# Optimization experiments

Hardware: AMD Instinct MI355X
Metric: run time of the kernel (lower is better)

## Reference

```python
import jax, jax.numpy as jnp
import numpy as np
from jax import lax

V_VOX, T_PTS, D, H, W = 12000, 35, 10, 200, 176
EPS = 1e-5


def _bn(x, g, b, axes, shape):
    m = x.mean(axes, keepdims=True)
    v = x.var(axes, keepdims=True)  # biased var, matches torch BN training stats
    return g.reshape(shape) * (x - m) * lax.rsqrt(v + EPS) + b.reshape(shape)


def _conv3d(x, w, b):
    y = lax.conv_general_dilated(x, w, (1, 1, 1), 'SAME',
                                 dimension_numbers=('NCDHW', 'OIDHW', 'NCDHW'))
    return y + b[None, :, None, None, None]


def _conv2d(x, w, b):
    y = lax.conv_general_dilated(x, w, (1, 1), 'SAME',
                                 dimension_numbers=('NCHW', 'OIHW', 'NCHW'))
    return y + b[None, :, None, None]


def setup_inputs() -> dict:
    key = jax.random.key(0)
    ks = jax.random.split(key, 12)
    voxels = jax.random.normal(ks[0], (1, V_VOX, T_PTS, 4), jnp.float32)
    # unique voxel coordinates (the torch loop overwrites on duplicates; unique avoids ambiguity)
    rng = np.random.default_rng(0)
    flat = rng.choice(D * H * W, size=V_VOX, replace=False)
    z = flat // (H * W); rem = flat % (H * W)
    coords = jnp.asarray(np.stack([z, rem // W, rem % W], axis=1), dtype=jnp.int32)
    s = 0.05
    p = dict(
        w_lin=jax.random.normal(ks[1], (32, 4), jnp.float32) * s,
        b_lin=jnp.zeros((32,), jnp.float32),
        g_bn0=jnp.ones((32,), jnp.float32), be_bn0=jnp.zeros((32,), jnp.float32),
        w_c3a=jax.random.normal(ks[2], (64, 32, 3, 3, 3), jnp.float32) * s,
        b_c3a=jnp.zeros((64,), jnp.float32),
        g_bn1=jnp.ones((64,), jnp.float32), be_bn1=jnp.zeros((64,), jnp.float32),
        w_c3b=jax.random.normal(ks[3], (64, 64, 3, 3, 3), jnp.float32) * s,
        b_c3b=jnp.zeros((64,), jnp.float32),
        g_bn2=jnp.ones((64,), jnp.float32), be_bn2=jnp.zeros((64,), jnp.float32),
        w_r1=jax.random.normal(ks[4], (128, 64, 3, 3), jnp.float32) * s,
        b_r1=jnp.zeros((128,), jnp.float32),
        w_r2=jax.random.normal(ks[5], (8, 128, 1, 1), jnp.float32) * s,
        b_r2=jnp.zeros((8,), jnp.float32),
    )
    return dict(voxels=voxels, coords=coords, **p)


def reference(voxels, coords, w_lin, b_lin, g_bn0, be_bn0,
              w_c3a, b_c3a, g_bn1, be_bn1, w_c3b, b_c3b, g_bn2, be_bn2,
              w_r1, b_r1, w_r2, b_r2):
    B, V, T, C = voxels.shape
    # SimpleVFE: linear -> BN1d (batch stats) -> relu -> max over points
    h = voxels.reshape(B * V * T, C) @ w_lin.T + b_lin          # [BVT,32]
    h = jax.nn.relu(_bn(h, g_bn0, be_bn0, 0, (1, 32)))
    feats = h.reshape(B, V, T, 32).max(axis=2)                  # [B,V,32]
    # fused scatter into dense volume (replaces per-voxel python loop)
    volume = jnp.zeros((B, 32, D, H, W), voxels.dtype)
    volume = volume.at[0, :, coords[:, 0], coords[:, 1], coords[:, 2]].set(feats[0])
    # 3D backbone
    x = jax.nn.relu(_bn(_conv3d(volume, w_c3a, b_c3a), g_bn1, be_bn1, (0, 2, 3, 4), (1, 64, 1, 1, 1)))
    x = jax.nn.relu(_bn(_conv3d(x, w_c3b, b_c3b), g_bn2, be_bn2, (0, 2, 3, 4), (1, 64, 1, 1, 1)))
    x = x.mean(axis=2)                                          # collapse depth -> [B,64,H,W]
    # RPN head
    out = _conv2d(jax.nn.relu(_conv2d(x, w_r1, b_r1)), w_r2, b_r2)  # [B,8,H,W]
    box = jnp.concatenate([out[:, 0:3], jnp.exp(out[:, 3:6]),
                           jnp.tanh(out[:, 6:7]), jax.nn.sigmoid(out[:, 7:8])], axis=1)
    return box
```

## Files before the change

kernel.cpp:

```cpp
#include <hip/hip_runtime.h>
#include <math.h>

#define V_VOX 12000
#define T_PTS 35
#define DD 10
#define HH 200
#define WW 176
#define EPSV 1e-5f

#define DP 12
#define HP 202
#define WP 178
#define PPLN (HP * WP)
#define PVOX (DP * PPLN)
#define NPIX (DD * HH * WW)
#define HWPIX (HH * WW)

typedef _Float16 half_t;
typedef _Float16 f16x8 __attribute__((ext_vector_type(8)));
typedef float f32x4 __attribute__((ext_vector_type(4)));

#define WPA_OFF 0
#define WPB_OFF 110592
#define WPR1_OFF 331776
#define STATS_OFF 479232
#define FEATS_OFF 483328
#define VOLP_OFF 2019328
#define X1P_OFF 29633536
#define Y_OFF 84861952
#define PLANE_OFF 129917952
#define R1OUT_OFF 134520320

#define S_BN0S 0
#define S_BN0Q 32
#define S_BN1S 64
#define S_BN1Q 128
#define S_BN2S 192
#define S_BN2Q 256
#define C0A 320
#define C0B 352
#define C1A 384
#define C1B 448
#define C2A 512
#define C2B 576

__device__ __forceinline__ void gload16(const half_t* g, half_t* l) {
    __builtin_amdgcn_global_load_lds(
        (const __attribute__((address_space(1))) void*)g,
        (__attribute__((address_space(3))) void*)l, 16, 0, 0);
}

__global__ void k_pack(const float* __restrict__ w, half_t* __restrict__ wp,
                       int IC, int NT, int OC) {
    int id = blockIdx.x * 256 + threadIdx.x;
    int OCT = OC >> 4, KH = IC >> 5;
    int total = NT * KH * OCT * 512;
    if (id >= total) return;
    int j = id & 7;
    int lane = (id >> 3) & 63;
    int rest = id >> 9;
    int ot = rest % OCT; rest /= OCT;
    int kh = rest % KH;
    int tap = rest / KH;
    int oc = ot * 16 + (lane & 15);
    int ic = kh * 32 + (lane >> 4) * 8 + j;
    wp[id] = (half_t)w[(oc * IC + ic) * NT + tap];
}

__global__ void k_vfe_stats(const float4* __restrict__ vox, const float* __restrict__ w_lin,
                            const float* __restrict__ b_lin, float* __restrict__ S) {
    int tid = blockIdx.x * 256 + threadIdx.x;
    int c = threadIdx.x & 31;
    float4 w = ((const float4*)w_lin)[c];
    float bl = b_lin[c];
    float s = 0.f, q = 0.f;
    const int np = V_VOX * T_PTS;
    int stride = gridDim.x * 8;
    for (int p = tid >> 5; p < np; p += stride) {
        float4 v = vox[p];
        float d = v.x * w.x + v.y * w.y + v.z * w.z + v.w * w.w + bl;
        s += d;
        q += d * d;
    }
    s += __shfl_xor(s, 32);
    q += __shfl_xor(q, 32);
    if ((threadIdx.x & 63) < 32) {
        atomicAdd(&S[S_BN0S + c], s);
        atomicAdd(&S[S_BN0Q + c], q);
    }
}

__global__ void k_bn_final(const float* __restrict__ ss, const float* __restrict__ sq,
                           const float* __restrict__ g, const float* __restrict__ be,
                           float* __restrict__ ca, float* __restrict__ cb, int C, float invN) {
    int c = threadIdx.x;
    if (c >= C) return;
    float m = ss[c] * invN;
    float v = sq[c] * invN - m * m;
    float a = g[c] * rsqrtf(v + EPSV);
    ca[c] = a;
    cb[c] = be[c] - m * a;
}

__global__ void k_vfe_max(const float4* __restrict__ vox, const float* __restrict__ w_lin,
                          const float* __restrict__ b_lin, const float* __restrict__ ca,
                          const float* __restrict__ cb, float* __restrict__ feats) {
    int id = blockIdx.x * 256 + threadIdx.x;
    if (id >= V_VOX * 32) return;
    int c = id & 31;
    int v = id >> 5;
    float4 w = ((const float4*)w_lin)[c];
    float bl = b_lin[c], A = ca[c], B = cb[c];
    float m = 0.f;
    for (int t = 0; t < T_PTS; t++) {
        float4 p = vox[v * T_PTS + t];
        float d = p.x * w.x + p.y * w.y + p.z * w.z + p.w * w.w + bl;
        m = fmaxf(m, A * d + B);
    }
    feats[id] = m;
}

__global__ void k_scatter(const float* __restrict__ feats, const int* __restrict__ coords,
                          half_t* __restrict__ volp) {
    int id = blockIdx.x * 256 + threadIdx.x;
    if (id >= V_VOX * 32) return;
    int c = id & 31;
    int v = id >> 5;
    int z = coords[v * 3 + 0];
    int y = coords[v * 3 + 1];
    int x = coords[v * 3 + 2];
    volp[(((z + 1) * HP + (y + 1)) * WP + (x + 1)) * 32 + c] = (half_t)feats[id];
}

template <int KH, int DZ, int OCTP, bool RELU, bool STATS>
__global__ __launch_bounds__(256, 4) void k_conv(const half_t* __restrict__ in,
                                                 size_t khstride,
                                                 const half_t* __restrict__ wp,
                                                 const float* __restrict__ bias,
                                                 half_t* __restrict__ out,
                                                 float* __restrict__ ssum,
                                                 float* __restrict__ ssq) {
    constexpr int OC = OCTP * 16;
    constexpr int NS = DZ * KH;
    __shared__ __align__(16) half_t tA[21 * 512];
    __shared__ __align__(16) half_t tB[18 * 512];

    const int tid = threadIdx.x;
    const int lane = tid & 63;
    const int wv = tid >> 6;
    const int x0 = blockIdx.x * 16;
    const int y0b = blockIdx.y * 16;
    const int bz = blockIdx.z;
    const int z0 = (DZ == 3) ? (bz >> 1) : 0;
    const int ocb = (DZ == 3) ? (bz & 1) * 2 : bz * 2;
    const int y0w = y0b + wv * 4;
    const bool valid = (y0w < HH);
    const int colc = lane & 15, grp = lane >> 4;

    unsigned gofsA[6];
#pragma unroll
    for (int i = 0; i < 6; ++i) {
        int run = wv + 4 * i;
        int c = run * 64 + lane;
        if (c > 1295) c = 1295;
        int pixhi = c >> 3, s = c & 7;
        int b = ((s >> 2) ^ (pixhi >> 1)) & 1;
        int q = ((s ^ b) & 1) | ((((s >> 1) ^ pixhi) & 1) << 1);
        int pix = pixhi * 2 + b;
        int row = pix / 18, px = pix - row * 18;
        int srow = y0b + row;
        if (srow > HP - 1) srow = HP - 1;
        gofsA[i] = (unsigned)((srow * WP + x0 + px) * 32 + q * 8);
    }

    f32x4 acc[4][2];
#pragma unroll
    for (int m = 0; m < 4; m++)
#pragma unroll
        for (int n = 0; n < 2; n++) acc[m][n] = (f32x4)(0.f);

#pragma unroll 1
    for (int s = 0; s < NS; ++s) {
        const int dz = s / KH, kh = s % KH;
        const half_t* sl = in + (size_t)kh * khstride
                           + (size_t)(z0 + dz) * (DZ == 3 ? (size_t)PPLN * 32 : 0);
#pragma unroll
        for (int i = 0; i < 6; ++i) {
            int run = wv + 4 * i;
            if (run < 21) gload16(sl + gofsA[i], &tA[run * 512]);
        }
#pragma unroll
        for (int i = 0; i < 5; ++i) {
            int r = wv + 4 * i;
            if (r < 18) {
                int tap = r >> 1, hf = r & 1;
                const half_t* g = wp + (((size_t)(dz * 9 + tap) * KH + kh) * OCTP + ocb + hf) * 512
                                  + lane * 8;
                gload16(g, &tB[r * 512]);
            }
        }
        asm volatile("s_waitcnt vmcnt(0)" ::: "memory");
        __syncthreads();

        if (valid) {
#pragma unroll
            for (int dx = 0; dx < 3; ++dx) {
                f16x8 Af[6];
#pragma unroll
                for (int r = 0; r < 6; ++r) {
                    int pix = (wv * 4 + r) * 18 + colc + dx;
                    int ah = ((pix << 5) | (grp << 3)) ^ ((pix & 7) << 3);
                    Af[r] = *(const f16x8*)&tA[ah];
                }
#pragma unroll
                for (int dy = 0; dy < 3; ++dy) {
                    f16x8 Bf[2];
#pragma unroll
                    for (int n = 0; n < 2; ++n)
                        Bf[n] = *(const f16x8*)&tB[((dy * 3 + dx) * 2 + n) * 512 + lane * 8];
#pragma unroll
                    for (int m = 0; m < 4; ++m)
#pragma unroll
                        for (int n = 0; n < 2; ++n)
                            acc[m][n] = __builtin_amdgcn_mfma_f32_16x16x32_f16(
                                Af[dy + m], Bf[n], acc[m][n], 0, 0, 0);
                }
            }
        }
        __syncthreads();
    }

    if (!valid) return;
#pragma unroll
    for (int n = 0; n < 2; ++n) {
        int oc = (ocb + n) * 16 + colc;
        float bv = bias[oc];
        float s = 0.f, q = 0.f;
#pragma unroll
        for (int m = 0; m < 4; ++m) {
            int yy = y0w + m;
#pragma unroll
            for (int i = 0; i < 4; ++i) {
                int xx = x0 + grp * 4 + i;
                float v = acc[m][n][i] + bv;
                if (STATS) { s += v; q += v * v; }
                float w = RELU ? fmaxf(v, 0.f) : v;
                out[((size_t)(z0 * HH + yy) * WW + xx) * OC + oc] = (half_t)w;
            }
        }
        if (STATS) {
            s += __shfl_xor(s, 16); s += __shfl_xor(s, 32);
            q += __shfl_xor(q, 16); q += __shfl_xor(q, 32);
            if (lane < 16) {
                atomicAdd(&ssum[oc], s);
                atomicAdd(&ssq[oc], q);
            }
        }
    }
}

__global__ void k_activate(const half_t* __restrict__ y1, const float* __restrict__ ca,
                           const float* __restrict__ cb, half_t* __restrict__ xp) {
    int id = blockIdx.x * 256 + threadIdx.x;
    if (id >= PVOX * 8) return;
    int c0 = (id & 7) * 8;
    int pix = id >> 3;
    int zp = pix / PPLN;
    int rem = pix - zp * PPLN;
    int yp = rem / WP;
    int xq = rem - yp * WP;
    f16x8 o;
    if (zp >= 1 && zp <= DD && yp >= 1 && yp <= HH && xq >= 1 && xq <= WW) {
        size_t p = ((size_t)((zp - 1) * HH + (yp - 1)) * WW + (xq - 1));
        f16x8 v = *(const f16x8*)(y1 + p * 64 + c0);
#pragma unroll
        for (int j = 0; j < 8; j++)
            o[j] = (half_t)fmaxf(ca[c0 + j] * (float)v[j] + cb[c0 + j], 0.f);
    } else {
#pragma unroll
        for (int j = 0; j < 8; j++) o[j] = (half_t)0.f;
    }
    int khp = c0 >> 5;
    *(f16x8*)(xp + (size_t)khp * PVOX * 32 + (size_t)pix * 32 + (c0 & 31)) = o;
}

__global__ void k_depthmean(const half_t* __restrict__ y2, const float* __restrict__ ca,
                            const float* __restrict__ cb, half_t* __restrict__ plane) {
    int id = blockIdx.x * 256 + threadIdx.x;
    int c = id & 63;
    int pix = id >> 6;
    int yp = pix / WP;
    int xq = pix - yp * WP;
    float val = 0.f;
    if (yp >= 1 && yp <= HH && xq >= 1 && xq <= WW) {
        float A = ca[c], B = cb[c], s = 0.f;
        const half_t* base = y2 + ((size_t)(yp - 1) * WW + (xq - 1)) * 64 + c;
#pragma unroll
        for (int z = 0; z < DD; z++)
            s += fmaxf(A * (float)base[(size_t)z * HWPIX * 64] + B, 0.f);
        val = s * 0.1f;
    }
    int khp = c >> 5;
    plane[(size_t)khp * PPLN * 32 + (size_t)pix * 32 + (c & 31)] = (half_t)val;
}

__global__ void k_r2(const half_t* __restrict__ r1o, const float* __restrict__ w,
                     const float* __restrict__ bias, float* __restrict__ outp) {
    __shared__ float wsm[1024];
    for (int i = threadIdx.x; i < 1024; i += 256) wsm[i] = w[i];
    __syncthreads();
    int p = blockIdx.x * 256 + threadIdx.x;
    if (p >= HWPIX) return;
    float acc[8];
#pragma unroll
    for (int o = 0; o < 8; o++) acc[o] = bias[o];
    const half_t* rb = r1o + (size_t)p * 128;
#pragma unroll 4
    for (int icb = 0; icb < 128; icb += 8) {
        f16x8 v = *(const f16x8*)(rb + icb);
#pragma unroll
        for (int j = 0; j < 8; j++) {
            float vv = (float)v[j];
#pragma unroll
            for (int o = 0; o < 8; o++) acc[o] += vv * wsm[o * 128 + icb + j];
        }
    }
    outp[0 * HWPIX + p] = acc[0];
    outp[1 * HWPIX + p] = acc[1];
    outp[2 * HWPIX + p] = acc[2];
    outp[3 * HWPIX + p] = expf(acc[3]);
    outp[4 * HWPIX + p] = expf(acc[4]);
    outp[5 * HWPIX + p] = expf(acc[5]);
    outp[6 * HWPIX + p] = tanhf(acc[6]);
    outp[7 * HWPIX + p] = 1.f / (1.f + expf(-acc[7]));
}

extern "C" void kernel_launch(void* const* d_in, const int* in_sizes, int n_in,
                              void* d_out, int out_size, void* d_ws, size_t ws_size,
                              hipStream_t stream) {
    const float4* voxels = (const float4*)d_in[0];
    const int* coords = (const int*)d_in[1];
    const float* w_lin = (const float*)d_in[2];
    const float* b_lin = (const float*)d_in[3];
    const float* g_bn0 = (const float*)d_in[4];
    const float* be_bn0 = (const float*)d_in[5];
    const float* w_c3a = (const float*)d_in[6];
    const float* b_c3a = (const float*)d_in[7];
    const float* g_bn1 = (const float*)d_in[8];
    const float* be_bn1 = (const float*)d_in[9];
    const float* w_c3b = (const float*)d_in[10];
    const float* b_c3b = (const float*)d_in[11];
    const float* g_bn2 = (const float*)d_in[12];
    const float* be_bn2 = (const float*)d_in[13];
    const float* w_r1 = (const float*)d_in[14];
    const float* b_r1 = (const float*)d_in[15];
    const float* w_r2 = (const float*)d_in[16];
    const float* b_r2 = (const float*)d_in[17];

    char* ws = (char*)d_ws;
    half_t* wpA = (half_t*)(ws + WPA_OFF);
    half_t* wpB = (half_t*)(ws + WPB_OFF);
    half_t* wpR1 = (half_t*)(ws + WPR1_OFF);
    float* S = (float*)(ws + STATS_OFF);
    float* feats = (float*)(ws + FEATS_OFF);
    half_t* volp = (half_t*)(ws + VOLP_OFF);
    half_t* x1p = (half_t*)(ws + X1P_OFF);
    half_t* Y = (half_t*)(ws + Y_OFF);
    half_t* plane = (half_t*)(ws + PLANE_OFF);
    half_t* r1out = (half_t*)(ws + R1OUT_OFF);
    float* outp = (float*)d_out;

    hipMemsetAsync(S, 0, 320 * sizeof(float), stream);
    hipMemsetAsync(volp, 0, (size_t)PVOX * 32 * sizeof(half_t), stream);

    k_pack<<<216, 256, 0, stream>>>(w_c3a, wpA, 32, 27, 64);
    k_pack<<<432, 256, 0, stream>>>(w_c3b, wpB, 64, 27, 64);
    k_pack<<<288, 256, 0, stream>>>(w_r1, wpR1, 64, 9, 128);

    k_vfe_stats<<<512, 256, 0, stream>>>(voxels, w_lin, b_lin, S);
    k_bn_final<<<1, 64, 0, stream>>>(S + S_BN0S, S + S_BN0Q, g_bn0, be_bn0,
                                     S + C0A, S + C0B, 32, 1.f / 420000.f);
    k_vfe_max<<<1500, 256, 0, stream>>>(voxels, w_lin, b_lin, S + C0A, S + C0B, feats);
    k_scatter<<<1500, 256, 0, stream>>>(feats, coords, volp);

    k_conv<1, 3, 4, false, true><<<dim3(11, 13, 20), 256, 0, stream>>>(
        volp, 0, wpA, b_c3a, Y, S + S_BN1S, S + S_BN1Q);
    k_bn_final<<<1, 64, 0, stream>>>(S + S_BN1S, S + S_BN1Q, g_bn1, be_bn1,
                                     S + C1A, S + C1B, 64, 1.f / 352000.f);
    k_activate<<<13484, 256, 0, stream>>>(Y, S + C1A, S + C1B, x1p);

    k_conv<2, 3, 4, false, true><<<dim3(11, 13, 20), 256, 0, stream>>>(
        x1p, (size_t)PVOX * 32, wpB, b_c3b, Y, S + S_BN2S, S + S_BN2Q);
    k_bn_final<<<1, 64, 0, stream>>>(S + S_BN2S, S + S_BN2Q, g_bn2, be_bn2,
                                     S + C2A, S + C2B, 64, 1.f / 352000.f);

    k_depthmean<<<8989, 256, 0, stream>>>(Y, S + C2A, S + C2B, plane);

    k_conv<2, 1, 8, true, false><<<dim3(11, 13, 4), 256, 0, stream>>>(
        plane, (size_t)PPLN * 32, wpR1, b_r1, r1out, nullptr, nullptr);
    k_r2<<<138, 256, 0, stream>>>(r1out, w_r2, b_r2, outp);
}
```

Baseline: 456.2 us.

## Switch implicit-GEMM conv to 32x32x16 MFMA with 512-thread blocks covering all output channels

The conv kernel now uses 32x32x16 f16 MFMA tiles instead of 16x16x32, with weights repacked into matching 32-channel, half-K fragments. Each block now has 8 waves split into y-groups and oc-groups and covers all 64 output channels for the 3D convs. The input tile is therefore loaded once per block instead of being re-fetched for each channel half. This aims to cut redundant activation loads and LDS reads per MFMA, at the cost of more LDS for weights, larger blocks and a different swizzle and epilogue mapping.

```diff
diff --git a/kernel.cpp b/kernel.cpp
--- a/kernel.cpp
+++ b/kernel.cpp
@@ -18,7 +18,7 @@
 
 typedef _Float16 half_t;
 typedef _Float16 f16x8 __attribute__((ext_vector_type(8)));
-typedef float f32x4 __attribute__((ext_vector_type(4)));
+typedef float f32x16 __attribute__((ext_vector_type(16)));
 
 #define WPA_OFF 0
 #define WPB_OFF 110592
@@ -53,17 +53,18 @@
 __global__ void k_pack(const float* __restrict__ w, half_t* __restrict__ wp,
                        int IC, int NT, int OC) {
     int id = blockIdx.x * 256 + threadIdx.x;
-    int OCT = OC >> 4, KH = IC >> 5;
-    int total = NT * KH * OCT * 512;
+    int OCT = OC >> 5, KH = IC >> 5;
+    int total = NT * KH * 2 * OCT * 512;
     if (id >= total) return;
     int j = id & 7;
     int lane = (id >> 3) & 63;
     int rest = id >> 9;
     int ot = rest % OCT; rest /= OCT;
+    int khf = rest & 1; rest >>= 1;
     int kh = rest % KH;
     int tap = rest / KH;
-    int oc = ot * 16 + (lane & 15);
-    int ic = kh * 32 + (lane >> 4) * 8 + j;
+    int oc = ot * 32 + (lane & 31);
+    int ic = kh * 32 + khf * 16 + (lane >> 5) * 8 + j;
     wp[id] = (half_t)w[(oc * IC + ic) * NT + tap];
 }
 
@@ -132,98 +133,97 @@
     volp[(((z + 1) * HP + (y + 1)) * WP + (x + 1)) * 32 + c] = (half_t)feats[id];
 }
 
-template <int KH, int DZ, int OCTP, bool RELU, bool STATS>
-__global__ __launch_bounds__(256, 4) void k_conv(const half_t* __restrict__ in,
+template <int KH, int DZ, int OCALL, bool RELU, bool STATS>
+__global__ __launch_bounds__(512, 4) void k_conv(const half_t* __restrict__ in,
                                                  size_t khstride,
                                                  const half_t* __restrict__ wp,
                                                  const float* __restrict__ bias,
                                                  half_t* __restrict__ out,
                                                  float* __restrict__ ssum,
                                                  float* __restrict__ ssq) {
-    constexpr int OC = OCTP * 16;
+    constexpr int OCT = OCALL / 32;
     constexpr int NS = DZ * KH;
-    __shared__ __align__(16) half_t tA[21 * 512];
-    __shared__ __align__(16) half_t tB[18 * 512];
+    __shared__ __align__(16) half_t tA[1296 * 8];
+    __shared__ __align__(16) half_t tB[36 * 512];
 
     const int tid = threadIdx.x;
     const int lane = tid & 63;
     const int wv = tid >> 6;
+    const int yg = wv >> 1;
+    const int og = wv & 1;
     const int x0 = blockIdx.x * 16;
     const int y0b = blockIdx.y * 16;
     const int bz = blockIdx.z;
-    const int z0 = (DZ == 3) ? (bz >> 1) : 0;
-    const int ocb = (DZ == 3) ? (bz & 1) * 2 : bz * 2;
-    const int y0w = y0b + wv * 4;
-    const bool valid = (y0w < HH);
-    const int colc = lane & 15, grp = lane >> 4;
-
-    unsigned gofsA[6];
-#pragma unroll
-    for (int i = 0; i < 6; ++i) {
-        int run = wv + 4 * i;
-        int c = run * 64 + lane;
-        if (c > 1295) c = 1295;
-        int pixhi = c >> 3, s = c & 7;
-        int b = ((s >> 2) ^ (pixhi >> 1)) & 1;
-        int q = ((s ^ b) & 1) | ((((s >> 1) ^ pixhi) & 1) << 1);
-        int pix = pixhi * 2 + b;
-        int row = pix / 18, px = pix - row * 18;
-        int srow = y0b + row;
-        if (srow > HP - 1) srow = HP - 1;
-        gofsA[i] = (unsigned)((srow * WP + x0 + px) * 32 + q * 8);
-    }
-
-    f32x4 acc[4][2];
-#pragma unroll
-    for (int m = 0; m < 4; m++)
-#pragma unroll
-        for (int n = 0; n < 2; n++) acc[m][n] = (f32x4)(0.f);
-
-#pragma unroll 1
-    for (int s = 0; s < NS; ++s) {
+    const int z0 = (DZ == 3) ? bz : 0;
+    const int ocb = (DZ == 3) ? 0 : bz * 2;
+    const bool valid = (y0b + yg * 4 < HH);
+    const int xl = lane & 15;
+    const int yrl = (lane >> 4) & 1;
+    const int kg = (lane >> 5) & 1;
+
+    int gofsA[3]; bool okA[3];
+#pragma unroll
+    for (int r = 0; r < 3; ++r) {
+        int c = tid + r * 512;
+        okA[r] = (c < 1296);
+        int cc = okA[r] ? c : 0;
+        int p0 = ((cc >> 2) ^ (cc >> 4)) & 1;
+        int p = ((cc >> 3) << 1) | p0;
+        int q = (cc & 3) ^ (p & 3);
+        int row = p / 18, px = p - row * 18;
+        int grow = y0b + row;
+        if (grow > HP - 1) grow = HP - 1;
+        gofsA[r] = (grow * WP + x0 + px) * 32 + q * 8;
+    }
+
+    f32x16 acc[2];
+#pragma unroll
+    for (int m = 0; m < 2; ++m) acc[m] = (f32x16)(0.f);
+
+    auto STAGE = [&](int s) {
         const int dz = s / KH, kh = s % KH;
         const half_t* sl = in + (size_t)kh * khstride
                            + (size_t)(z0 + dz) * (DZ == 3 ? (size_t)PPLN * 32 : 0);
 #pragma unroll
-        for (int i = 0; i < 6; ++i) {
-            int run = wv + 4 * i;
-            if (run < 21) gload16(sl + gofsA[i], &tA[run * 512]);
-        }
-#pragma unroll
-        for (int i = 0; i < 5; ++i) {
-            int r = wv + 4 * i;
-            if (r < 18) {
-                int tap = r >> 1, hf = r & 1;
-                const half_t* g = wp + (((size_t)(dz * 9 + tap) * KH + kh) * OCTP + ocb + hf) * 512
-                                  + lane * 8;
-                gload16(g, &tB[r * 512]);
+        for (int r = 0; r < 3; ++r)
+            if (okA[r]) gload16(sl + gofsA[r], &tA[(size_t)(tid + r * 512) * 8]);
+#pragma unroll
+        for (int r = 0; r < 5; ++r) {
+            int c = tid + r * 512;
+            if (c < 2304) {
+                int u = c >> 6;
+                int tl = u >> 2, khf = (u >> 1) & 1, ot = u & 1;
+                const half_t* g = wp + ((((size_t)(dz * 9 + tl) * KH + kh) * 2 + khf) * OCT
+                                        + ocb + ot) * 512 + lane * 8;
+                gload16(g, &tB[(size_t)u * 512 + lane * 8]);
             }
         }
+    };
+
+#pragma unroll 1
+    for (int s = 0; s < NS; ++s) {
+        STAGE(s);
         asm volatile("s_waitcnt vmcnt(0)" ::: "memory");
         __syncthreads();
 
         if (valid) {
 #pragma unroll
-            for (int dx = 0; dx < 3; ++dx) {
-                f16x8 Af[6];
-#pragma unroll
-                for (int r = 0; r < 6; ++r) {
-                    int pix = (wv * 4 + r) * 18 + colc + dx;
-                    int ah = ((pix << 5) | (grp << 3)) ^ ((pix & 7) << 3);
-                    Af[r] = *(const f16x8*)&tA[ah];
-                }
-#pragma unroll
-                for (int dy = 0; dy < 3; ++dy) {
-                    f16x8 Bf[2];
-#pragma unroll
-                    for (int n = 0; n < 2; ++n)
-                        Bf[n] = *(const f16x8*)&tB[((dy * 3 + dx) * 2 + n) * 512 + lane * 8];
-#pragma unroll
-                    for (int m = 0; m < 4; ++m)
-#pragma unroll
-                        for (int n = 0; n < 2; ++n)
-                            acc[m][n] = __builtin_amdgcn_mfma_f32_16x16x32_f16(
-                                Af[dy + m], Bf[n], acc[m][n], 0, 0, 0);
+            for (int khalf = 0; khalf < 2; ++khalf) {
+#pragma unroll
+                for (int dx = 0; dx < 3; ++dx) {
+#pragma unroll
+                    for (int dy = 0; dy < 3; ++dy) {
+                        int u = ((dy * 3 + dx) * 2 + khalf) * 2 + og;
+                        f16x8 Bf = *(const f16x8*)&tB[u * 512 + lane * 8];
+#pragma unroll
+                        for (int m = 0; m < 2; ++m) {
+                            int p = (yg * 4 + dy + 2 * m + yrl) * 18 + dx + xl;
+                            int ph = ((p << 6) | ((khalf * 2 + kg) << 4)) ^ ((p & 7) << 4);
+                            f16x8 Af = *(const f16x8*)((const char*)tA + ph);
+                            acc[m] = __builtin_amdgcn_mfma_f32_32x32x16_f16(
+                                Af, Bf, acc[m], 0, 0, 0);
+                        }
+                    }
                 }
             }
         }
@@ -231,30 +231,28 @@
     }
 
     if (!valid) return;
-#pragma unroll
-    for (int n = 0; n < 2; ++n) {
-        int oc = (ocb + n) * 16 + colc;
-        float bv = bias[oc];
-        float s = 0.f, q = 0.f;
-#pragma unroll
-        for (int m = 0; m < 4; ++m) {
-            int yy = y0w + m;
-#pragma unroll
-            for (int i = 0; i < 4; ++i) {
-                int xx = x0 + grp * 4 + i;
-                float v = acc[m][n][i] + bv;
-                if (STATS) { s += v; q += v * v; }
-                float w = RELU ? fmaxf(v, 0.f) : v;
-                out[((size_t)(z0 * HH + yy) * WW + xx) * OC + oc] = (half_t)w;
-            }
+    float sreg = 0.f, qreg = 0.f;
+    int oc = (ocb + og) * 32 + (lane & 31);
+    float bv = bias[oc];
+#pragma unroll
+    for (int m = 0; m < 2; ++m) {
+#pragma unroll
+        for (int reg = 0; reg < 16; ++reg) {
+            int rp = (reg & 3) + 8 * (reg >> 2) + 4 * kg;
+            int xx = x0 + (rp & 15);
+            int yy = y0b + yg * 4 + 2 * m + (rp >> 4);
+            float v = acc[m][reg] + bv;
+            if (STATS) { sreg += v; qreg += v * v; }
+            float w = RELU ? fmaxf(v, 0.f) : v;
+            out[((size_t)(z0 * HH + yy) * WW + xx) * OCALL + oc] = (half_t)w;
         }
-        if (STATS) {
-            s += __shfl_xor(s, 16); s += __shfl_xor(s, 32);
-            q += __shfl_xor(q, 16); q += __shfl_xor(q, 32);
-            if (lane < 16) {
-                atomicAdd(&ssum[oc], s);
-                atomicAdd(&ssq[oc], q);
-            }
+    }
+    if (STATS) {
+        sreg += __shfl_xor(sreg, 32);
+        qreg += __shfl_xor(qreg, 32);
+        if (lane < 32) {
+            atomicAdd(&ssum[oc], sreg);
+            atomicAdd(&ssq[oc], qreg);
         }
     }
 }
@@ -383,20 +381,20 @@
     k_vfe_max<<<1500, 256, 0, stream>>>(voxels, w_lin, b_lin, S + C0A, S + C0B, feats);
     k_scatter<<<1500, 256, 0, stream>>>(feats, coords, volp);
 
-    k_conv<1, 3, 4, false, true><<<dim3(11, 13, 20), 256, 0, stream>>>(
+    k_conv<1, 3, 64, false, true><<<dim3(11, 13, 10), 512, 0, stream>>>(
         volp, 0, wpA, b_c3a, Y, S + S_BN1S, S + S_BN1Q);
     k_bn_final<<<1, 64, 0, stream>>>(S + S_BN1S, S + S_BN1Q, g_bn1, be_bn1,
                                      S + C1A, S + C1B, 64, 1.f / 352000.f);
     k_activate<<<13484, 256, 0, stream>>>(Y, S + C1A, S + C1B, x1p);
 
-    k_conv<2, 3, 4, false, true><<<dim3(11, 13, 20), 256, 0, stream>>>(
+    k_conv<2, 3, 64, false, true><<<dim3(11, 13, 10), 512, 0, stream>>>(
         x1p, (size_t)PVOX * 32, wpB, b_c3b, Y, S + S_BN2S, S + S_BN2Q);
     k_bn_final<<<1, 64, 0, stream>>>(S + S_BN2S, S + S_BN2Q, g_bn2, be_bn2,
                                      S + C2A, S + C2B, 64, 1.f / 352000.f);
 
     k_depthmean<<<8989, 256, 0, stream>>>(Y, S + C2A, S + C2B, plane);
 
-    k_conv<2, 1, 8, true, false><<<dim3(11, 13, 4), 256, 0, stream>>>(
+    k_conv<2, 1, 128, true, false><<<dim3(11, 13, 2), 512, 0, stream>>>(
         plane, (size_t)PPLN * 32, wpR1, b_r1, r1out, nullptr, nullptr);
     k_r2<<<138, 256, 0, stream>>>(r1out, w_r2, b_r2, outp);
 }
```

After: 468.4 us. +2.7%, slower.
